# Optimization experiments

Hardware: AMD Instinct MI355X
Metric: run time of the kernel (lower is better)

Reference implementation:

```python
import jax, jax.numpy as jnp
import numpy as np

EPS = 1e-5


def _conv1x1(w, x):
    # w: [O, C, 1, 1], x: [B, C, H, W] -> [B, O, H, W]
    return jnp.einsum('oc,bchw->bohw', w[:, :, 0, 0], x)


def _bn_train(y, g, b):
    # BatchNorm2d in training mode: batch statistics over (B, H, W)
    m = y.mean(axis=(0, 2, 3), keepdims=True)
    v = y.var(axis=(0, 2, 3), keepdims=True)
    return (y - m) * jax.lax.rsqrt(v + EPS) * g[None, :, None, None] + b[None, :, None, None]


def setup_inputs() -> dict:
    key = jax.random.key(0)
    ks = jax.random.split(key, 8)
    B, C, H, W = 16, 512, 32, 32
    width, heads, hd, out_ch = 128, 4, 32, 512  # out_chans*expansion = 512
    return {
        'x': jax.random.normal(ks[0], (B, C, H, W), jnp.float32),
        'conv1_w': jax.random.normal(ks[1], (width, C, 1, 1), jnp.float32) * 0.05,
        'bn1_g': jnp.ones((width,), jnp.float32),
        'bn1_b': jnp.zeros((width,), jnp.float32),
        'qkv_w': jax.random.normal(ks[2], (3 * width, width, 1, 1), jnp.float32) * 0.05,
        'rw': jax.random.normal(ks[3], (1, heads, hd, 1, W), jnp.float32),
        'rh': jax.random.normal(ks[4], (1, heads, hd, H, 1), jnp.float32),
        'conv2_w': jax.random.normal(ks[5], (out_ch, width, 1, 1), jnp.float32) * 0.05,
        'bn2_g': jnp.ones((out_ch,), jnp.float32),
        'bn2_b': jnp.zeros((out_ch,), jnp.float32),
    }


def reference(x, conv1_w, bn1_g, bn1_b, qkv_w, rw, rh, conv2_w, bn2_g, bn2_b):
    B, C, H, W = x.shape
    heads = rw.shape[1]
    width = qkv_w.shape[1]
    hd = width // heads
    scale = hd ** (-0.5)
    N = H * W

    identity = x
    # conv1 = BaseConv: 1x1 conv (no bias) + BN + ReLU
    y = jax.nn.relu(_bn_train(_conv1x1(conv1_w, x), bn1_g, bn1_b))

    # Attention with relative position bias
    qkv = _conv1x1(qkv_w, y)                       # [B, 3*width, H, W]
    qkv = qkv.reshape(B, 3, heads, hd, N)          # split channels as (3, heads, hd)
    q, k, v = qkv[:, 0], qkv[:, 1], qkv[:, 2]      # each [B, heads, hd, N]

    attn_content = jnp.einsum('bhdn,bhdm->bhnm', q, k) * scale  # [B, heads, N, N]
    r = (rw + rh).reshape(heads, hd, N)                          # [heads, hd, N]
    attn_position = jnp.einsum('bhdn,hdm->bhnm', q, r) * scale
    attn = jax.nn.softmax(attn_content + attn_position, axis=-1)
    out = jnp.einsum('bhnm,bhdm->bhdn', attn, v)   # [B, heads, hd, N]
    y = out.reshape(B, width, H, W)

    # conv2 + BN, residual add, ReLU (stride==1: no pooling, no down_sample)
    y = _bn_train(_conv1x1(conv2_w, y), bn2_g, bn2_b)
    y = y + identity
    return jax.nn.relu(y)
```

## Files before the change

### kernel.cpp

```cpp
#include <hip/hip_runtime.h>
#include <cstddef>
#include <cstdint>

constexpr int BATCH = 16;
constexpr int NQ    = 1024;
constexpr float QSCALE = 0.17677669529663687f * 1.4426950408889634f;

typedef __attribute__((ext_vector_type(8))) short bf8;
typedef __attribute__((ext_vector_type(4))) float f32x4;
typedef __attribute__((ext_vector_type(2))) unsigned short us2;
typedef __attribute__((ext_vector_type(4))) unsigned short us4;
typedef __attribute__((ext_vector_type(8))) unsigned short us8;

__device__ inline unsigned short f2bf(float x) {
  union { float f; uint32_t u; } c{x};
  uint32_t r = c.u + 0x7fffu + ((c.u >> 16) & 1u);
  return (unsigned short)(r >> 16);
}
__device__ inline float b2f(unsigned short v) {
  union { uint32_t u; float f; } c{(uint32_t)v << 16};
  return c.f;
}
__device__ inline float fast_exp2(float x) {
#if __has_builtin(__builtin_amdgcn_exp2f)
  return __builtin_amdgcn_exp2f(x);
#else
  return exp2f(x);
#endif
}

__global__ __launch_bounds__(256) void k_wcvt(const float* __restrict__ w1,
                                              const float* __restrict__ wq,
                                              const float* __restrict__ w2,
                                              unsigned short* __restrict__ o1,
                                              unsigned short* __restrict__ oq,
                                              unsigned short* __restrict__ o2) {
  int idx = (blockIdx.x * 256 + threadIdx.x) * 8;
  const float* s; unsigned short* d; int off;
  if (idx < 65536)        { s = w1; d = o1; off = idx; }
  else if (idx < 114688)  { s = wq; d = oq; off = idx - 65536; }
  else                    { s = w2; d = o2; off = idx - 114688; }
  float4 a = *(const float4*)(s + off);
  float4 b = *(const float4*)(s + off + 4);
  us8 o = {f2bf(a.x), f2bf(a.y), f2bf(a.z), f2bf(a.w),
           f2bf(b.x), f2bf(b.y), f2bf(b.z), f2bf(b.w)};
  *(us8*)(d + off) = o;
}

__global__ __launch_bounds__(256) void k_conv1(const float* __restrict__ x,
                                               const unsigned short* __restrict__ W,
                                               unsigned short* __restrict__ y1T,
                                               float* __restrict__ pS1,
                                               float* __restrict__ pQ1) {
  constexpr int BS = 68;
  __shared__ unsigned short Bl[32 * BS];
  __shared__ float Sl[128], Ql[128];

  const int bb = blockIdx.z;
  const int n0 = blockIdx.x * 32;
  const int tid = threadIdx.x, lane = tid & 63;
  const int wm = tid >> 6;
  const int i = lane & 15, g = lane >> 4;

  const int kb = tid >> 3;
  const int nb = tid & 7;

  f32x4 acc[2][2];
#pragma unroll
  for (int a = 0; a < 2; ++a)
#pragma unroll
    for (int b = 0; b < 2; ++b) acc[a][b] = {0.f, 0.f, 0.f, 0.f};

  float4 rv[2];
#pragma unroll
  for (int r = 0; r < 2; ++r)
    rv[r] = *(const float4*)(x + (((size_t)(bb * 512 + kb * 2 + r)) << 10) + n0 + nb * 4);

  for (int s = 0; s < 8; ++s) {
    bf8 wf[2][2];
#pragma unroll
    for (int b = 0; b < 2; ++b)
#pragma unroll
      for (int h = 0; h < 2; ++h)
        wf[b][h] = *(const bf8*)(W + (size_t)(wm * 32 + b * 16 + i) * 512 + s * 64 + h * 32 + g * 8);

    __syncthreads();
#pragma unroll
    for (int j = 0; j < 4; ++j) {
      us2 pk = {f2bf((&rv[0].x)[j]), f2bf((&rv[1].x)[j])};
      *(us2*)&Bl[(nb * 4 + j) * BS + kb * 2] = pk;
    }
    __syncthreads();

    if (s < 7) {
#pragma unroll
      for (int r = 0; r < 2; ++r)
        rv[r] = *(const float4*)(x + (((size_t)(bb * 512 + (s + 1) * 64 + kb * 2 + r)) << 10) + n0 + nb * 4);
    }

#pragma unroll
    for (int h = 0; h < 2; ++h) {
      bf8 af[2];
#pragma unroll
      for (int a = 0; a < 2; ++a)
        af[a] = *(const bf8*)&Bl[(a * 16 + i) * BS + h * 32 + g * 8];
#pragma unroll
      for (int a = 0; a < 2; ++a)
#pragma unroll
        for (int b = 0; b < 2; ++b)
          acc[a][b] = __builtin_amdgcn_mfma_f32_16x16x32_bf16(wf[b][h], af[a], acc[a][b], 0, 0, 0);
    }
  }

#pragma unroll
  for (int a = 0; a < 2; ++a)
#pragma unroll
    for (int b = 0; b < 2; ++b) {
      const int n = n0 + a * 16 + i;
      const int c = wm * 32 + b * 16 + 4 * g;
      us4 pk = {f2bf(acc[a][b][0]), f2bf(acc[a][b][1]), f2bf(acc[a][b][2]), f2bf(acc[a][b][3])};
      *(us4*)(y1T + ((size_t)(bb << 10) + n) * 128 + c) = pk;
    }

#pragma unroll
  for (int b = 0; b < 2; ++b) {
    float sb[4], qb[4];
#pragma unroll
    for (int r = 0; r < 4; ++r) {
      float v0 = b2f(f2bf(acc[0][b][r]));
      float v1 = b2f(f2bf(acc[1][b][r]));
      sb[r] = v0 + v1;
      qb[r] = v0 * v0 + v1 * v1;
    }
#pragma unroll
    for (int o = 1; o < 16; o <<= 1) {
#pragma unroll
      for (int r = 0; r < 4; ++r) {
        sb[r] += __shfl_xor(sb[r], o);
        qb[r] += __shfl_xor(qb[r], o);
      }
    }
    if (i == 0) {
#pragma unroll
      for (int r = 0; r < 4; ++r) {
        const int c = wm * 32 + b * 16 + 4 * g + r;
        Sl[c] = sb[r];
        Ql[c] = qb[r];
      }
    }
  }

  __syncthreads();
  const int blk = bb * 32 + blockIdx.x;
  if (tid < 128) {
    pS1[(size_t)tid * 512 + blk] = Sl[tid];
    pQ1[(size_t)tid * 512 + blk] = Ql[tid];
  }
}

__global__ __launch_bounds__(64) void k_bnfin1(const float* __restrict__ pS1,
                                               const float* __restrict__ pQ1,
                                               const float* __restrict__ g,
                                               const float* __restrict__ be,
                                               float* __restrict__ scl,
                                               float* __restrict__ sht) {
  const int c = blockIdx.x, t = threadIdx.x;
  float S = 0.f, Q = 0.f;
#pragma unroll
  for (int k = 0; k < 8; ++k) {
    S += pS1[(size_t)c * 512 + t + k * 64];
    Q += pQ1[(size_t)c * 512 + t + k * 64];
  }
#pragma unroll
  for (int o = 32; o > 0; o >>= 1) {
    S += __shfl_down(S, o);
    Q += __shfl_down(Q, o);
  }
  if (t == 0) {
    const float inv_n = 1.f / 16384.f;
    const float mean = S * inv_n, var = Q * inv_n - mean * mean;
    const float sc = rsqrtf(var + 1e-5f) * g[c];
    scl[c] = sc;
    sht[c] = be[c] - mean * sc;
  }
}

__global__ __launch_bounds__(256) void k_qkv(const unsigned short* __restrict__ W,
                                             const unsigned short* __restrict__ Bact,
                                             const float* __restrict__ scl,
                                             const float* __restrict__ sht,
                                             const float* __restrict__ rw,
                                             const float* __restrict__ rh,
                                             unsigned short* __restrict__ out0,
                                             unsigned short* __restrict__ out1,
                                             unsigned short* __restrict__ out2) {
  constexpr int BS = 136;
  __shared__ unsigned short Blds[128 * BS];
  __shared__ float scl_s[128], sht_s[128];

  const int bb = blockIdx.z, half = blockIdx.y;
  const int n0 = blockIdx.x * 128;
  const int tid = threadIdx.x, lane = tid & 63, wv = tid >> 6;
  const int wn = wv & 1, wm = wv >> 1;
  const int i = lane & 15, g = lane >> 4;

  const unsigned short* Bp = Bact + ((size_t)bb * NQ + n0) * 128;

  const int sn = tid >> 1;
  const int sk = (tid & 1) * 8;

  if (tid < 128) { scl_s[tid] = scl[tid]; sht_s[tid] = sht[tid]; }

  auto loadw = [&](bf8 (&wf)[2][4], int typ) {
    const int m0 = typ * 128 + half * 64;
#pragma unroll
    for (int b = 0; b < 2; ++b)
#pragma unroll
      for (int h = 0; h < 4; ++h)
        wf[b][h] = *(const bf8*)(W + (size_t)(m0 + wm * 32 + b * 16 + i) * 128 + h * 32 + g * 8);
  };

  bf8 wf0[2][4], wf1[2][4];
  loadw(wf0, 0);
  __syncthreads();

#pragma unroll
  for (int p = 0; p < 8; ++p) {
    us8 v = *(const us8*)(Bp + (size_t)sn * 128 + sk + p * 16);
    const int kb = sk + p * 16;
    float scv[8], shv[8];
    *(float4*)scv = *(const float4*)&scl_s[kb];
    *(float4*)(scv + 4) = *(const float4*)&scl_s[kb + 4];
    *(float4*)shv = *(const float4*)&sht_s[kb];
    *(float4*)(shv + 4) = *(const float4*)&sht_s[kb + 4];
#pragma unroll
    for (int j = 0; j < 8; ++j)
      v[j] = f2bf(fmaxf(fmaf(b2f(v[j]), scv[j], shv[j]), 0.f));
    *(us8*)(&Blds[sn * BS + sk + p * 16]) = v;
  }
  __syncthreads();

  f32x4 acc[4][2];

  auto gemmWA = [&](bf8 (&wf)[2][4]) {
#pragma unroll
    for (int a = 0; a < 4; ++a)
#pragma unroll
      for (int b = 0; b < 2; ++b) acc[a][b] = {0.f, 0.f, 0.f, 0.f};
#pragma unroll
    for (int h = 0; h < 4; ++h) {
      bf8 af[4];
#pragma unroll
      for (int a = 0; a < 4; ++a)
        af[a] = *(const bf8*)&Blds[(wn * 64 + a * 16 + i) * BS + h * 32 + g * 8];
#pragma unroll
      for (int a = 0; a < 4; ++a)
#pragma unroll
        for (int b = 0; b < 2; ++b)
          acc[a][b] = __builtin_amdgcn_mfma_f32_16x16x32_bf16(wf[b][h], af[a], acc[a][b], 0, 0, 0);
    }
  };
  auto gemmAW = [&](bf8 (&wf)[2][4]) {
#pragma unroll
    for (int a = 0; a < 4; ++a)
#pragma unroll
      for (int b = 0; b < 2; ++b) acc[a][b] = {0.f, 0.f, 0.f, 0.f};
#pragma unroll
    for (int h = 0; h < 4; ++h) {
      bf8 af[4];
#pragma unroll
      for (int a = 0; a < 4; ++a)
        af[a] = *(const bf8*)&Blds[(wn * 64 + a * 16 + i) * BS + h * 32 + g * 8];
#pragma unroll
      for (int a = 0; a < 4; ++a)
#pragma unroll
        for (int b = 0; b < 2; ++b)
          acc[a][b] = __builtin_amdgcn_mfma_f32_16x16x32_bf16(af[a], wf[b][h], acc[a][b], 0, 0, 0);
    }
  };

  loadw(wf1, 1);
  gemmWA(wf0);
#pragma unroll
  for (int a = 0; a < 4; ++a)
#pragma unroll
    for (int b = 0; b < 2; ++b) {
      const int n = n0 + wn * 64 + a * 16 + i;
      const int c = half * 64 + wm * 32 + b * 16 + 4 * g;
      const int hh = c >> 5, d = c & 31;
      us4 pk = {f2bf(acc[a][b][0] * QSCALE), f2bf(acc[a][b][1] * QSCALE),
                f2bf(acc[a][b][2] * QSCALE), f2bf(acc[a][b][3] * QSCALE)};
      *(us4*)(out0 + (((size_t)(bb * 4 + hh) << 10) + n) * 32 + d) = pk;
    }

  loadw(wf0, 2);
  gemmWA(wf1);
#pragma unroll
  for (int a = 0; a < 4; ++a)
#pragma unroll
    for (int b = 0; b < 2; ++b) {
      const int n = n0 + wn * 64 + a * 16 + i;
      const int c = half * 64 + wm * 32 + b * 16 + 4 * g;
      const int hh = c >> 5, d = c & 31;
      const int wcol = n & 31, hrow = n >> 5;
      float vv[4];
#pragma unroll
      for (int r = 0; r < 4; ++r)
        vv[r] = acc[a][b][r] + rw[(c + r) * 32 + wcol] + rh[(c + r) * 32 + hrow];
      us4 pk = {f2bf(vv[0]), f2bf(vv[1]), f2bf(vv[2]), f2bf(vv[3])};
      *(us4*)(out1 + (((size_t)(bb * 4 + hh) << 10) + n) * 32 + d) = pk;
    }

  gemmAW(wf0);
#pragma unroll
  for (int a = 0; a < 4; ++a)
#pragma unroll
    for (int b = 0; b < 2; ++b) {
      const int c = half * 64 + wm * 32 + b * 16 + i;
      const int nb = n0 + wn * 64 + a * 16 + 4 * g;
      const int hh = c >> 5, dd = c & 31;
      us4 pk = {f2bf(acc[a][b][0]), f2bf(acc[a][b][1]), f2bf(acc[a][b][2]), f2bf(acc[a][b][3])};
      *(us4*)(out2 + (((size_t)(bb * 4 + hh) * 32 + dd) << 10) + nb) = pk;
    }
}

__global__ __launch_bounds__(256) void k_attn_part(const unsigned short* __restrict__ qs,
                                                   const unsigned short* __restrict__ kt,
                                                   const unsigned short* __restrict__ vt,
                                                   float* __restrict__ po,
                                                   float* __restrict__ pm,
                                                   float* __restrict__ pl) {
  const int bh   = blockIdx.y;
  const int part = blockIdx.z;
  const int tid  = threadIdx.x;
  const int lane = tid & 63;
  const int wv   = tid >> 6;
  const int i    = lane & 15;
  const int g    = lane >> 4;
  const int n0w  = blockIdx.x * 128 + wv * 32;

  __shared__ unsigned short Ks[64 * 56];
  __shared__ unsigned short Vt[32 * 72];

  const bf8 qfA = *(const bf8*)(qs + ((size_t)bh * NQ + n0w + i) * 32 + g * 8);
  const bf8 qfB = *(const bf8*)(qs + ((size_t)bh * NQ + n0w + 16 + i) * 32 + g * 8);

  f32x4 o0A = {0.f,0.f,0.f,0.f}, o1A = {0.f,0.f,0.f,0.f};
  f32x4 o0B = {0.f,0.f,0.f,0.f}, o1B = {0.f,0.f,0.f,0.f};
  float mA = -1e30f, lA = 0.f, mB = -1e30f, lB = 0.f;

  const unsigned short* kb = kt + (size_t)bh * NQ * 32;
  const unsigned short* vb = vt + (size_t)bh * 32 * NQ;

  const int skey = tid >> 2, sds = (tid & 3) * 8;
  const int svd  = tid >> 3, svn = (tid & 7) * 8;

  const int kbeg = part * 512, kend = kbeg + 512;

  bf8 kvld = *(const bf8*)(kb + (size_t)(kbeg + skey) * 32 + sds);
  bf8 vvld = *(const bf8*)(vb + (size_t)svd * NQ + kbeg + svn);

  for (int k0 = kbeg; k0 < kend; k0 += 64) {
    __syncthreads();
    *(bf8*)&Ks[skey * 56 + sds] = kvld;
    *(bf8*)&Vt[svd * 72 + svn]  = vvld;
    __syncthreads();
    if (k0 + 64 < kend) {
      kvld = *(const bf8*)(kb + (size_t)(k0 + 64 + skey) * 32 + sds);
      vvld = *(const bf8*)(vb + (size_t)svd * NQ + (k0 + 64) + svn);
    }

    const f32x4 zero = {0.f,0.f,0.f,0.f};
    f32x4 stA[4], stB[4];
#pragma unroll
    for (int t = 0; t < 4; ++t) {
      bf8 kf = *(const bf8*)&Ks[(t * 16 + i) * 56 + g * 8];
      stA[t] = __builtin_amdgcn_mfma_f32_16x16x32_bf16(kf, qfA, zero, 0, 0, 0);
      stB[t] = __builtin_amdgcn_mfma_f32_16x16x32_bf16(kf, qfB, zero, 0, 0, 0);
    }

    unsigned int pkA[4][2], pkB[4][2];
    {
      float tmax = stA[0][0];
#pragma unroll
      for (int t = 0; t < 4; ++t)
#pragma unroll
        for (int r = 0; r < 4; ++r) tmax = fmaxf(tmax, stA[t][r]);
      tmax = fmaxf(tmax, __shfl_xor(tmax, 16));
      tmax = fmaxf(tmax, __shfl_xor(tmax, 32));
      const float mn = fmaxf(mA, tmax);
      const float corr = fast_exp2(mA - mn);
      mA = mn;
      float ps = 0.f;
#pragma unroll
      for (int t = 0; t < 4; ++t) {
        float p0 = fast_exp2(stA[t][0] - mn);
        float p1 = fast_exp2(stA[t][1] - mn);
        float p2 = fast_exp2(stA[t][2] - mn);
        float p3 = fast_exp2(stA[t][3] - mn);
        ps += (p0 + p1) + (p2 + p3);
        unsigned int pa, pb;
        asm("v_cvt_pk_bf16_f32 %0, %1, %2" : "=v"(pa) : "v"(p0), "v"(p1));
        asm("v_cvt_pk_bf16_f32 %0, %1, %2" : "=v"(pb) : "v"(p2), "v"(p3));
        pkA[t][0] = pa; pkA[t][1] = pb;
      }
      ps += __shfl_xor(ps, 16);
      ps += __shfl_xor(ps, 32);
      lA = lA * corr + ps;
#pragma unroll
      for (int r = 0; r < 4; ++r) { o0A[r] *= corr; o1A[r] *= corr; }
    }
    {
      float tmax = stB[0][0];
#pragma unroll
      for (int t = 0; t < 4; ++t)
#pragma unroll
        for (int r = 0; r < 4; ++r) tmax = fmaxf(tmax, stB[t][r]);
      tmax = fmaxf(tmax, __shfl_xor(tmax, 16));
      tmax = fmaxf(tmax, __shfl_xor(tmax, 32));
      const float mn = fmaxf(mB, tmax);
      const float corr = fast_exp2(mB - mn);
      mB = mn;
      float ps = 0.f;
#pragma unroll
      for (int t = 0; t < 4; ++t) {
        float p0 = fast_exp2(stB[t][0] - mn);
        float p1 = fast_exp2(stB[t][1] - mn);
        float p2 = fast_exp2(stB[t][2] - mn);
        float p3 = fast_exp2(stB[t][3] - mn);
        ps += (p0 + p1) + (p2 + p3);
        unsigned int pa, pb;
        asm("v_cvt_pk_bf16_f32 %0, %1, %2" : "=v"(pa) : "v"(p0), "v"(p1));
        asm("v_cvt_pk_bf16_f32 %0, %1, %2" : "=v"(pb) : "v"(p2), "v"(p3));
        pkB[t][0] = pa; pkB[t][1] = pb;
      }
      ps += __shfl_xor(ps, 16);
      ps += __shfl_xor(ps, 32);
      lB = lB * corr + ps;
#pragma unroll
      for (int r = 0; r < 4; ++r) { o0B[r] *= corr; o1B[r] *= corr; }
    }

    const int src0 = ((g & 1) << 5) + i;
    const int src1 = src0 + 16;
    const bool hi = (g >= 2);
#pragma unroll
    for (int s = 0; s < 2; ++s) {
      int a0 = __shfl((int)pkA[2 * s][0], src0);
      int a1 = __shfl((int)pkA[2 * s][1], src0);
      int a2 = __shfl((int)pkA[2 * s][0], src1);
      int a3 = __shfl((int)pkA[2 * s][1], src1);
      int b0 = __shfl((int)pkA[2 * s + 1][0], src0);
      int b1 = __shfl((int)pkA[2 * s + 1][1], src0);
      int b2 = __shfl((int)pkA[2 * s + 1][0], src1);
      int b3 = __shfl((int)pkA[2 * s + 1][1], src1);
      union { int d[4]; bf8 v; } pfA;
      pfA.d[0] = hi ? b0 : a0;
      pfA.d[1] = hi ? b1 : a1;
      pfA.d[2] = hi ? b2 : a2;
      pfA.d[3] = hi ? b3 : a3;
      int c0 = __shfl((int)pkB[2 * s][0], src0);
      int c1 = __shfl((int)pkB[2 * s][1], src0);
      int c2 = __shfl((int)pkB[2 * s][0], src1);
      int c3 = __shfl((int)pkB[2 * s][1], src1);
      int d0 = __shfl((int)pkB[2 * s + 1][0], src0);
      int d1 = __shfl((int)pkB[2 * s + 1][1], src0);
      int d2 = __shfl((int)pkB[2 * s + 1][0], src1);
      int d3 = __shfl((int)pkB[2 * s + 1][1], src1);
      union { int d[4]; bf8 v; } pfB;
      pfB.d[0] = hi ? d0 : c0;
      pfB.d[1] = hi ? d1 : c1;
      pfB.d[2] = hi ? d2 : c2;
      pfB.d[3] = hi ? d3 : c3;
      bf8 vf0 = *(const bf8*)&Vt[(i)      * 72 + s * 32 + g * 8];
      bf8 vf1 = *(const bf8*)&Vt[(16 + i) * 72 + s * 32 + g * 8];
      o0A = __builtin_amdgcn_mfma_f32_16x16x32_bf16(vf0, pfA.v, o0A, 0, 0, 0);
      o1A = __builtin_amdgcn_mfma_f32_16x16x32_bf16(vf1, pfA.v, o1A, 0, 0, 0);
      o0B = __builtin_amdgcn_mfma_f32_16x16x32_bf16(vf0, pfB.v, o0B, 0, 0, 0);
      o1B = __builtin_amdgcn_mfma_f32_16x16x32_bf16(vf1, pfB.v, o1B, 0, 0, 0);
    }
  }

  const size_t pb = ((size_t)(part * 64 + bh) << 10);
  float* dA = po + (pb + n0w + i) * 32 + 4 * g;
  float* dB = po + (pb + n0w + 16 + i) * 32 + 4 * g;
  *(f32x4*)dA        = o0A;
  *(f32x4*)(dA + 16) = o1A;
  *(f32x4*)dB        = o0B;
  *(f32x4*)(dB + 16) = o1B;
  if (g == 0) {
    pm[pb + n0w + i]      = mA;
    pl[pb + n0w + i]      = lA;
    pm[pb + n0w + 16 + i] = mB;
    pl[pb + n0w + 16 + i] = lB;
  }
}

__global__ __launch_bounds__(256) void k_attn_comb(const float* __restrict__ po,
                                                   const float* __restrict__ pm,
                                                   const float* __restrict__ pl,
                                                   float* __restrict__ aoT) {
  const int bh = blockIdx.y;
  const int q  = blockIdx.x * 64 + (threadIdx.x >> 2);
  const int dc = (threadIdx.x & 3) * 8;

  const size_t p0 = ((size_t)bh << 10) + q;
  const size_t p1 = ((size_t)(64 + bh) << 10) + q;

  const float m0 = pm[p0], m1 = pm[p1];
  const float l0 = pl[p0], l1 = pl[p1];
  const float M  = fmaxf(m0, m1);
  const float w0 = fast_exp2(m0 - M);
  const float w1 = fast_exp2(m1 - M);
  const float inv = 1.f / (w0 * l0 + w1 * l1);
  const float c0 = w0 * inv, c1 = w1 * inv;

  f32x4 a0 = *(const f32x4*)(po + p0 * 32 + dc);
  f32x4 a1 = *(const f32x4*)(po + p0 * 32 + dc + 4);
  f32x4 b0 = *(const f32x4*)(po + p1 * 32 + dc);
  f32x4 b1 = *(const f32x4*)(po + p1 * 32 + dc + 4);
  f32x4 o0, o1;
#pragma unroll
  for (int r = 0; r < 4; ++r) {
    o0[r] = a0[r] * c0 + b0[r] * c1;
    o1[r] = a1[r] * c0 + b1[r] * c1;
  }

  float* dst = aoT + (((size_t)(bh >> 2) << 10) + q) * 128 + (bh & 3) * 32 + dc;
  *(f32x4*)dst       = o0;
  *(f32x4*)(dst + 4) = o1;
}

__global__ __launch_bounds__(256) void k_stat2(const unsigned short* __restrict__ W,
                                               const float* __restrict__ Aof,
                                               float* __restrict__ pBS,
                                               float* __restrict__ pBQ) {
  constexpr int BS = 264;
  __shared__ unsigned short Blds[64 * BS];
  __shared__ float Sl[256], Ql[256];
  const int bb = blockIdx.z;
  const int mh = blockIdx.y;
  const int n0 = blockIdx.x * 64;
  const int tid = threadIdx.x, lane = tid & 63, wv = tid >> 6;
  const int wn = wv & 1, wm = wv >> 1;
  const int i = lane & 15, g = lane >> 4;

  Sl[tid] = 0.f; Ql[tid] = 0.f;

  const int sn = tid >> 2, sk = (tid & 3) * 32;
  const float* src = Aof + (((size_t)(bb << 10)) + n0 + sn) * 128 + sk;
#pragma unroll
  for (int p = 0; p < 4; ++p) {
    float4 f0 = *(const float4*)(src + p * 8);
    float4 f1 = *(const float4*)(src + p * 8 + 4);
    float fv[8] = {f0.x, f0.y, f0.z, f0.w, f1.x, f1.y, f1.z, f1.w};
    us8 hi, lo;
#pragma unroll
    for (int j = 0; j < 8; ++j) {
      unsigned short h16 = f2bf(fv[j]);
      hi[j] = h16;
      lo[j] = f2bf(fv[j] - b2f(h16));
    }
    *(us8*)&Blds[sn * BS + sk + p * 8]       = hi;
    *(us8*)&Blds[sn * BS + 128 + sk + p * 8] = lo;
  }
  __syncthreads();

  auto loadw = [&](bf8 (&wf)[2][4], int lp) {
    const int mt = mh * 4 + lp;
#pragma unroll
    for (int b = 0; b < 2; ++b)
#pragma unroll
      for (int h = 0; h < 4; ++h)
        wf[b][h] = *(const bf8*)(W + (size_t)(mt * 64 + wm * 32 + b * 16 + i) * 128 + h * 32 + g * 8);
  };

  auto step = [&](bf8 (&wf)[2][4], int lp) {
    f32x4 acc[2][2];
#pragma unroll
    for (int a = 0; a < 2; ++a)
#pragma unroll
      for (int b = 0; b < 2; ++b) acc[a][b] = {0.f, 0.f, 0.f, 0.f};
#pragma unroll
    for (int h = 0; h < 4; ++h) {
      bf8 ah[2], al[2];
#pragma unroll
      for (int a = 0; a < 2; ++a) {
        ah[a] = *(const bf8*)&Blds[(wn * 32 + a * 16 + i) * BS + h * 32 + g * 8];
        al[a] = *(const bf8*)&Blds[(wn * 32 + a * 16 + i) * BS + 128 + h * 32 + g * 8];
      }
#pragma unroll
      for (int a = 0; a < 2; ++a)
#pragma unroll
        for (int b = 0; b < 2; ++b) {
          acc[a][b] = __builtin_amdgcn_mfma_f32_16x16x32_bf16(ah[a], wf[b][h], acc[a][b], 0, 0, 0);
          acc[a][b] = __builtin_amdgcn_mfma_f32_16x16x32_bf16(al[a], wf[b][h], acc[a][b], 0, 0, 0);
        }
    }
#pragma unroll
    for (int b = 0; b < 2; ++b) {
      float s = 0.f, q = 0.f;
#pragma unroll
      for (int a = 0; a < 2; ++a)
#pragma unroll
        for (int r = 0; r < 4; ++r) {
          float v = acc[a][b][r];
          s += v; q += v * v;
        }
      s += __shfl_xor(s, 16); s += __shfl_xor(s, 32);
      q += __shfl_xor(q, 16); q += __shfl_xor(q, 32);
      if ((lane & 48) == 0) {
        const int cl = lp * 64 + wm * 32 + b * 16 + i;
        atomicAdd(&Sl[cl], s);
        atomicAdd(&Ql[cl], q);
      }
    }
  };

  bf8 wfA[2][4], wfB[2][4];
  loadw(wfA, 0);
  loadw(wfB, 1);
  step(wfA, 0);
  loadw(wfA, 2);
  step(wfB, 1);
  loadw(wfB, 3);
  step(wfA, 2);
  step(wfB, 3);

  __syncthreads();
  const int pidx = bb * 16 + blockIdx.x;
  pBS[(size_t)(mh * 256 + tid) * 256 + pidx] = Sl[tid];
  pBQ[(size_t)(mh * 256 + tid) * 256 + pidx] = Ql[tid];
}

__global__ __launch_bounds__(64) void k_bnfin2(const float* __restrict__ pBS,
                                               const float* __restrict__ pBQ,
                                               const float* __restrict__ g,
                                               const float* __restrict__ be,
                                               float* __restrict__ scl,
                                               float* __restrict__ sht) {
  const int c = blockIdx.x, t = threadIdx.x;
  float S = 0.f, Q = 0.f;
#pragma unroll
  for (int k = 0; k < 4; ++k) {
    S += pBS[(size_t)c * 256 + t + k * 64];
    Q += pBQ[(size_t)c * 256 + t + k * 64];
  }
#pragma unroll
  for (int o = 32; o > 0; o >>= 1) {
    S += __shfl_down(S, o);
    Q += __shfl_down(Q, o);
  }
  if (t == 0) {
    const float inv_n = 1.f / 16384.f;
    const float mean = S * inv_n, var = Q * inv_n - mean * mean;
    const float sc = rsqrtf(var + 1e-5f) * g[c];
    scl[c] = sc;
    sht[c] = be[c] - mean * sc;
  }
}

__global__ __launch_bounds__(256) void k_final2(const unsigned short* __restrict__ W,
                                                const float* __restrict__ Aof,
                                                const float* __restrict__ x,
                                                const float* __restrict__ scl2,
                                                const float* __restrict__ sht2,
                                                float* __restrict__ out) {
  constexpr int BS = 264;
  __shared__ unsigned short Blds[64 * BS];
  __shared__ float scl_s[256], sht_s[256];
  const int bb = blockIdx.z;
  const int mh = blockIdx.y;
  const int n0 = blockIdx.x * 64;
  const int tid = threadIdx.x, lane = tid & 63, wv = tid >> 6;
  const int wn = wv & 1, wm = wv >> 1;
  const int i = lane & 15, g = lane >> 4;

  scl_s[tid] = scl2[mh * 256 + tid];
  sht_s[tid] = sht2[mh * 256 + tid];

  const int sn = tid >> 2, sk = (tid & 3) * 32;
  const float* src = Aof + (((size_t)(bb << 10)) + n0 + sn) * 128 + sk;
#pragma unroll
  for (int p = 0; p < 4; ++p) {
    float4 f0 = *(const float4*)(src + p * 8);
    float4 f1 = *(const float4*)(src + p * 8 + 4);
    float fv[8] = {f0.x, f0.y, f0.z, f0.w, f1.x, f1.y, f1.z, f1.w};
    us8 hi, lo;
#pragma unroll
    for (int j = 0; j < 8; ++j) {
      unsigned short h16 = f2bf(fv[j]);
      hi[j] = h16;
      lo[j] = f2bf(fv[j] - b2f(h16));
    }
    *(us8*)&Blds[sn * BS + sk + p * 8]       = hi;
    *(us8*)&Blds[sn * BS + 128 + sk + p * 8] = lo;
  }
  __syncthreads();

  auto loadw = [&](bf8 (&wf)[2][4], int lp) {
    const int mt = mh * 4 + lp;
#pragma unroll
    for (int b = 0; b < 2; ++b)
#pragma unroll
      for (int h = 0; h < 4; ++h)
        wf[b][h] = *(const bf8*)(W + (size_t)(mt * 64 + wm * 32 + b * 16 + i) * 128 + h * 32 + g * 8);
  };

  auto step = [&](bf8 (&wf)[2][4], int lp) {
    const int mt = mh * 4 + lp;
    f32x4 acc[2][2];
#pragma unroll
    for (int a = 0; a < 2; ++a)
#pragma unroll
      for (int b = 0; b < 2; ++b) acc[a][b] = {0.f, 0.f, 0.f, 0.f};
#pragma unroll
    for (int h = 0; h < 4; ++h) {
      bf8 ah[2], al[2];
#pragma unroll
      for (int a = 0; a < 2; ++a) {
        ah[a] = *(const bf8*)&Blds[(wn * 32 + a * 16 + i) * BS + h * 32 + g * 8];
        al[a] = *(const bf8*)&Blds[(wn * 32 + a * 16 + i) * BS + 128 + h * 32 + g * 8];
      }
#pragma unroll
      for (int a = 0; a < 2; ++a)
#pragma unroll
        for (int b = 0; b < 2; ++b) {
          acc[a][b] = __builtin_amdgcn_mfma_f32_16x16x32_bf16(ah[a], wf[b][h], acc[a][b], 0, 0, 0);
          acc[a][b] = __builtin_amdgcn_mfma_f32_16x16x32_bf16(al[a], wf[b][h], acc[a][b], 0, 0, 0);
        }
    }
#pragma unroll
    for (int a = 0; a < 2; ++a)
#pragma unroll
      for (int b = 0; b < 2; ++b) {
        const int c = mt * 64 + wm * 32 + b * 16 + i;
        const int cl = lp * 64 + wm * 32 + b * 16 + i;
        const int nb = n0 + wn * 32 + a * 16 + 4 * g;
        const float sc = scl_s[cl], sh = sht_s[cl];
        const size_t off = (((size_t)(bb * 512 + c)) << 10) + nb;
        float4 xv = *(const float4*)(x + off);
        f32x4 o;
        o[0] = fmaxf(acc[a][b][0] * sc + sh + xv.x, 0.f);
        o[1] = fmaxf(acc[a][b][1] * sc + sh + xv.y, 0.f);
        o[2] = fmaxf(acc[a][b][2] * sc + sh + xv.z, 0.f);
        o[3] = fmaxf(acc[a][b][3] * sc + sh + xv.w, 0.f);
        *(f32x4*)(out + off) = o;
      }
  };

  bf8 wfA[2][4], wfB[2][4];
  loadw(wfA, 0);
  loadw(wfB, 1);
  step(wfA, 0);
  loadw(wfA, 2);
  step(wfB, 1);
  loadw(wfB, 3);
  step(wfA, 2);
  step(wfB, 3);
}

extern "C" void kernel_launch(void* const* d_in, const int* in_sizes, int n_in,
                              void* d_out, int out_size, void* d_ws, size_t ws_size,
                              hipStream_t stream) {
  (void)in_sizes; (void)n_in; (void)out_size; (void)ws_size;
  const float* x    = (const float*)d_in[0];
  const float* w1   = (const float*)d_in[1];
  const float* g1   = (const float*)d_in[2];
  const float* b1   = (const float*)d_in[3];
  const float* wqkv = (const float*)d_in[4];
  const float* rw   = (const float*)d_in[5];
  const float* rh   = (const float*)d_in[6];
  const float* w2   = (const float*)d_in[7];
  const float* g2   = (const float*)d_in[8];
  const float* b2   = (const float*)d_in[9];
  float* out = (float*)d_out;
  char* base = (char*)d_ws;

  float*          aoT = (float*)(base);
  unsigned short* y1T = (unsigned short*)(base + (8u  << 20));
  unsigned short* qs  = (unsigned short*)(base + (12u << 20));
  unsigned short* kt  = (unsigned short*)(base + (16u << 20));
  unsigned short* vt  = (unsigned short*)(base + (20u << 20));
  unsigned short* wb1 = (unsigned short*)(base + (24u << 20));
  unsigned short* wbq = wb1 + 65536;
  unsigned short* wb2 = wbq + 49152;
  float* pS1  = (float*)(base + (25u << 20));
  float* pQ1  = pS1 + 65536;
  float* pBS  = pQ1 + 65536;
  float* pBQ  = pBS + 131072;
  float* scl1 = pBQ + 131072;
  float* sht1 = scl1 + 128;
  float* scl2 = sht1 + 128;
  float* sht2 = scl2 + 512;
  float* po   = (float*)(base + (32u << 20));
  float* pm   = (float*)(base + (48u << 20));
  float* pl   = pm + 131072;

  k_wcvt<<<88, 256, 0, stream>>>(w1, wqkv, w2, wb1, wbq, wb2);
  k_conv1<<<dim3(32, 1, BATCH), 256, 0, stream>>>(x, wb1, y1T, pS1, pQ1);
  k_bnfin1<<<128, 64, 0, stream>>>(pS1, pQ1, g1, b1, scl1, sht1);
  k_qkv<<<dim3(8, 2, BATCH), 256, 0, stream>>>(wbq, y1T, scl1, sht1,
                                               rw, rh, qs, kt, vt);
  k_attn_part<<<dim3(NQ / 128, BATCH * 4, 2), 256, 0, stream>>>(qs, kt, vt, po, pm, pl);
  k_attn_comb<<<dim3(16, BATCH * 4), 256, 0, stream>>>(po, pm, pl, aoT);
  k_stat2<<<dim3(16, 2, BATCH), 256, 0, stream>>>(wb2, aoT, pBS, pBQ);
  k_bnfin2<<<512, 64, 0, stream>>>(pBS, pBQ, g2, b2, scl2, sht2);
  k_final2<<<dim3(16, 2, BATCH), 256, 0, stream>>>(wb2, aoT, x, scl2, sht2, out);
}
```

Measured before the change: 103.3 us.

## Double-buffer K/V tiles in attention and fuse split-combine into conv2 kernels

```diff
diff --git a/kernel.cpp b/kernel.cpp
--- a/kernel.cpp
+++ b/kernel.cpp
@@ -339,8 +339,8 @@
   const int g    = lane >> 4;
   const int n0w  = blockIdx.x * 128 + wv * 32;
 
-  __shared__ unsigned short Ks[64 * 56];
-  __shared__ unsigned short Vt[32 * 72];
+  __shared__ unsigned short Ks[2][64 * 56];
+  __shared__ unsigned short Vt[2][32 * 72];
 
   const bf8 qfA = *(const bf8*)(qs + ((size_t)bh * NQ + n0w + i) * 32 + g * 8);
   const bf8 qfB = *(const bf8*)(qs + ((size_t)bh * NQ + n0w + 16 + i) * 32 + g * 8);
@@ -355,29 +355,32 @@
   const int skey = tid >> 2, sds = (tid & 3) * 8;
   const int svd  = tid >> 3, svn = (tid & 7) * 8;
 
-  const int kbeg = part * 512, kend = kbeg + 512;
+  const int kbeg = part * 512;
 
   bf8 kvld = *(const bf8*)(kb + (size_t)(kbeg + skey) * 32 + sds);
   bf8 vvld = *(const bf8*)(vb + (size_t)svd * NQ + kbeg + svn);
-
-  for (int k0 = kbeg; k0 < kend; k0 += 64) {
-    __syncthreads();
-    *(bf8*)&Ks[skey * 56 + sds] = kvld;
-    *(bf8*)&Vt[svd * 72 + svn]  = vvld;
-    __syncthreads();
-    if (k0 + 64 < kend) {
-      kvld = *(const bf8*)(kb + (size_t)(k0 + 64 + skey) * 32 + sds);
-      vvld = *(const bf8*)(vb + (size_t)svd * NQ + (k0 + 64) + svn);
+  *(bf8*)&Ks[0][skey * 56 + sds] = kvld;
+  *(bf8*)&Vt[0][svd * 72 + svn]  = vvld;
+  __syncthreads();
+
+  for (int it = 0; it < 8; ++it) {
+    const int cur = it & 1, nxt = cur ^ 1;
+    if (it < 7) {
+      const int k0n = kbeg + (it + 1) * 64;
+      kvld = *(const bf8*)(kb + (size_t)(k0n + skey) * 32 + sds);
+      vvld = *(const bf8*)(vb + (size_t)svd * NQ + k0n + svn);
     }
 
     const f32x4 zero = {0.f,0.f,0.f,0.f};
     f32x4 stA[4], stB[4];
+    __builtin_amdgcn_s_setprio(1);
 #pragma unroll
     for (int t = 0; t < 4; ++t) {
-      bf8 kf = *(const bf8*)&Ks[(t * 16 + i) * 56 + g * 8];
+      bf8 kf = *(const bf8*)&Ks[cur][(t * 16 + i) * 56 + g * 8];
       stA[t] = __builtin_amdgcn_mfma_f32_16x16x32_bf16(kf, qfA, zero, 0, 0, 0);
       stB[t] = __builtin_amdgcn_mfma_f32_16x16x32_bf16(kf, qfB, zero, 0, 0, 0);
     }
+    __builtin_amdgcn_s_setprio(0);
 
     unsigned int pkA[4][2], pkB[4][2];
     {
@@ -444,6 +447,7 @@
     const int src0 = ((g & 1) << 5) + i;
     const int src1 = src0 + 16;
     const bool hi = (g >= 2);
+    __builtin_amdgcn_s_setprio(1);
 #pragma unroll
     for (int s = 0; s < 2; ++s) {
       int a0 = __shfl((int)pkA[2 * s][0], src0);
@@ -472,13 +476,20 @@
       pfB.d[1] = hi ? d1 : c1;
       pfB.d[2] = hi ? d2 : c2;
       pfB.d[3] = hi ? d3 : c3;
-      bf8 vf0 = *(const bf8*)&Vt[(i)      * 72 + s * 32 + g * 8];
-      bf8 vf1 = *(const bf8*)&Vt[(16 + i) * 72 + s * 32 + g * 8];
+      bf8 vf0 = *(const bf8*)&Vt[cur][(i)      * 72 + s * 32 + g * 8];
+      bf8 vf1 = *(const bf8*)&Vt[cur][(16 + i) * 72 + s * 32 + g * 8];
       o0A = __builtin_amdgcn_mfma_f32_16x16x32_bf16(vf0, pfA.v, o0A, 0, 0, 0);
       o1A = __builtin_amdgcn_mfma_f32_16x16x32_bf16(vf1, pfA.v, o1A, 0, 0, 0);
       o0B = __builtin_amdgcn_mfma_f32_16x16x32_bf16(vf0, pfB.v, o0B, 0, 0, 0);
       o1B = __builtin_amdgcn_mfma_f32_16x16x32_bf16(vf1, pfB.v, o1B, 0, 0, 0);
     }
+    __builtin_amdgcn_s_setprio(0);
+
+    if (it < 7) {
+      *(bf8*)&Ks[nxt][skey * 56 + sds] = kvld;
+      *(bf8*)&Vt[nxt][svd * 72 + svn]  = vvld;
+    }
+    __syncthreads();
   }
 
   const size_t pb = ((size_t)(part * 64 + bh) << 10);
@@ -496,43 +507,10 @@
   }
 }
 
-__global__ __launch_bounds__(256) void k_attn_comb(const float* __restrict__ po,
-                                                   const float* __restrict__ pm,
-                                                   const float* __restrict__ pl,
-                                                   float* __restrict__ aoT) {
-  const int bh = blockIdx.y;
-  const int q  = blockIdx.x * 64 + (threadIdx.x >> 2);
-  const int dc = (threadIdx.x & 3) * 8;
-
-  const size_t p0 = ((size_t)bh << 10) + q;
-  const size_t p1 = ((size_t)(64 + bh) << 10) + q;
-
-  const float m0 = pm[p0], m1 = pm[p1];
-  const float l0 = pl[p0], l1 = pl[p1];
-  const float M  = fmaxf(m0, m1);
-  const float w0 = fast_exp2(m0 - M);
-  const float w1 = fast_exp2(m1 - M);
-  const float inv = 1.f / (w0 * l0 + w1 * l1);
-  const float c0 = w0 * inv, c1 = w1 * inv;
-
-  f32x4 a0 = *(const f32x4*)(po + p0 * 32 + dc);
-  f32x4 a1 = *(const f32x4*)(po + p0 * 32 + dc + 4);
-  f32x4 b0 = *(const f32x4*)(po + p1 * 32 + dc);
-  f32x4 b1 = *(const f32x4*)(po + p1 * 32 + dc + 4);
-  f32x4 o0, o1;
-#pragma unroll
-  for (int r = 0; r < 4; ++r) {
-    o0[r] = a0[r] * c0 + b0[r] * c1;
-    o1[r] = a1[r] * c0 + b1[r] * c1;
-  }
-
-  float* dst = aoT + (((size_t)(bh >> 2) << 10) + q) * 128 + (bh & 3) * 32 + dc;
-  *(f32x4*)dst       = o0;
-  *(f32x4*)(dst + 4) = o1;
-}
-
 __global__ __launch_bounds__(256) void k_stat2(const unsigned short* __restrict__ W,
-                                               const float* __restrict__ Aof,
+                                               const float* __restrict__ po,
+                                               const float* __restrict__ pm,
+                                               const float* __restrict__ pl,
                                                float* __restrict__ pBS,
                                                float* __restrict__ pBQ) {
   constexpr int BS = 264;
@@ -547,22 +525,43 @@
 
   Sl[tid] = 0.f; Ql[tid] = 0.f;
 
-  const int sn = tid >> 2, sk = (tid & 3) * 32;
-  const float* src = Aof + (((size_t)(bb << 10)) + n0 + sn) * 128 + sk;
-#pragma unroll
-  for (int p = 0; p < 4; ++p) {
-    float4 f0 = *(const float4*)(src + p * 8);
-    float4 f1 = *(const float4*)(src + p * 8 + 4);
-    float fv[8] = {f0.x, f0.y, f0.z, f0.w, f1.x, f1.y, f1.z, f1.w};
-    us8 hi, lo;
-#pragma unroll
-    for (int j = 0; j < 8; ++j) {
-      unsigned short h16 = f2bf(fv[j]);
-      hi[j] = h16;
-      lo[j] = f2bf(fv[j] - b2f(h16));
-    }
-    *(us8*)&Blds[sn * BS + sk + p * 8]       = hi;
-    *(us8*)&Blds[sn * BS + 128 + sk + p * 8] = lo;
+  {
+    const int sn = tid >> 2, sk = (tid & 3) * 32;
+    const int h  = tid & 3;
+    const int n  = n0 + sn;
+    const size_t q0 = (((size_t)(bb * 4 + h)) << 10) + n;
+    const size_t q1 = (((size_t)(64 + bb * 4 + h)) << 10) + n;
+    const float m0 = pm[q0], m1 = pm[q1];
+    const float l0 = pl[q0], l1 = pl[q1];
+    const float M  = fmaxf(m0, m1);
+    const float w0 = fast_exp2(m0 - M);
+    const float w1 = fast_exp2(m1 - M);
+    const float inv = 1.f / (w0 * l0 + w1 * l1);
+    const float c0 = w0 * inv, c1 = w1 * inv;
+    const float* s0 = po + q0 * 32;
+    const float* s1 = po + q1 * 32;
+#pragma unroll
+    for (int p = 0; p < 4; ++p) {
+      f32x4 a0 = *(const f32x4*)(s0 + p * 8);
+      f32x4 a1 = *(const f32x4*)(s0 + p * 8 + 4);
+      f32x4 b0 = *(const f32x4*)(s1 + p * 8);
+      f32x4 b1 = *(const f32x4*)(s1 + p * 8 + 4);
+      float fv[8];
+#pragma unroll
+      for (int r = 0; r < 4; ++r) {
+        fv[r]     = a0[r] * c0 + b0[r] * c1;
+        fv[4 + r] = a1[r] * c0 + b1[r] * c1;
+      }
+      us8 hi, lo;
+#pragma unroll
+      for (int j = 0; j < 8; ++j) {
+        unsigned short h16 = f2bf(fv[j]);
+        hi[j] = h16;
+        lo[j] = f2bf(fv[j] - b2f(h16));
+      }
+      *(us8*)&Blds[sn * BS + sk + p * 8]       = hi;
+      *(us8*)&Blds[sn * BS + 128 + sk + p * 8] = lo;
+    }
   }
   __syncthreads();
 
@@ -661,7 +660,9 @@
 }
 
 __global__ __launch_bounds__(256) void k_final2(const unsigned short* __restrict__ W,
-                                                const float* __restrict__ Aof,
+                                                const float* __restrict__ po,
+                                                const float* __restrict__ pm,
+                                                const float* __restrict__ pl,
                                                 const float* __restrict__ x,
                                                 const float* __restrict__ scl2,
                                                 const float* __restrict__ sht2,
@@ -679,22 +680,43 @@
   scl_s[tid] = scl2[mh * 256 + tid];
   sht_s[tid] = sht2[mh * 256 + tid];
 
-  const int sn = tid >> 2, sk = (tid & 3) * 32;
-  const float* src = Aof + (((size_t)(bb << 10)) + n0 + sn) * 128 + sk;
-#pragma unroll
-  for (int p = 0; p < 4; ++p) {
-    float4 f0 = *(const float4*)(src + p * 8);
-    float4 f1 = *(const float4*)(src + p * 8 + 4);
-    float fv[8] = {f0.x, f0.y, f0.z, f0.w, f1.x, f1.y, f1.z, f1.w};
-    us8 hi, lo;
-#pragma unroll
-    for (int j = 0; j < 8; ++j) {
-      unsigned short h16 = f2bf(fv[j]);
-      hi[j] = h16;
-      lo[j] = f2bf(fv[j] - b2f(h16));
-    }
-    *(us8*)&Blds[sn * BS + sk + p * 8]       = hi;
-    *(us8*)&Blds[sn * BS + 128 + sk + p * 8] = lo;
+  {
+    const int sn = tid >> 2, sk = (tid & 3) * 32;
+    const int h  = tid & 3;
+    const int n  = n0 + sn;
+    const size_t q0 = (((size_t)(bb * 4 + h)) << 10) + n;
+    const size_t q1 = (((size_t)(64 + bb * 4 + h)) << 10) + n;
+    const float m0 = pm[q0], m1 = pm[q1];
+    const float l0 = pl[q0], l1 = pl[q1];
+    const float M  = fmaxf(m0, m1);
+    const float w0 = fast_exp2(m0 - M);
+    const float w1 = fast_exp2(m1 - M);
+    const float inv = 1.f / (w0 * l0 + w1 * l1);
+    const float c0 = w0 * inv, c1 = w1 * inv;
+    const float* s0 = po + q0 * 32;
+    const float* s1 = po + q1 * 32;
+#pragma unroll
+    for (int p = 0; p < 4; ++p) {
+      f32x4 a0 = *(const f32x4*)(s0 + p * 8);
+      f32x4 a1 = *(const f32x4*)(s0 + p * 8 + 4);
+      f32x4 b0 = *(const f32x4*)(s1 + p * 8);
+      f32x4 b1 = *(const f32x4*)(s1 + p * 8 + 4);
+      float fv[8];
+#pragma unroll
+      for (int r = 0; r < 4; ++r) {
+        fv[r]     = a0[r] * c0 + b0[r] * c1;
+        fv[4 + r] = a1[r] * c0 + b1[r] * c1;
+      }
+      us8 hi, lo;
+#pragma unroll
+      for (int j = 0; j < 8; ++j) {
+        unsigned short h16 = f2bf(fv[j]);
+        hi[j] = h16;
+        lo[j] = f2bf(fv[j] - b2f(h16));
+      }
+      *(us8*)&Blds[sn * BS + sk + p * 8]       = hi;
+      *(us8*)&Blds[sn * BS + 128 + sk + p * 8] = lo;
+    }
   }
   __syncthreads();
 
@@ -777,7 +799,6 @@
   float* out = (float*)d_out;
   char* base = (char*)d_ws;
 
-  float*          aoT = (float*)(base);
   unsigned short* y1T = (unsigned short*)(base + (8u  << 20));
   unsigned short* qs  = (unsigned short*)(base + (12u << 20));
   unsigned short* kt  = (unsigned short*)(base + (16u << 20));
@@ -803,8 +824,7 @@
   k_qkv<<<dim3(8, 2, BATCH), 256, 0, stream>>>(wbq, y1T, scl1, sht1,
                                                rw, rh, qs, kt, vt);
   k_attn_part<<<dim3(NQ / 128, BATCH * 4, 2), 256, 0, stream>>>(qs, kt, vt, po, pm, pl);
-  k_attn_comb<<<dim3(16, BATCH * 4), 256, 0, stream>>>(po, pm, pl, aoT);
-  k_stat2<<<dim3(16, 2, BATCH), 256, 0, stream>>>(wb2, aoT, pBS, pBQ);
+  k_stat2<<<dim3(16, 2, BATCH), 256, 0, stream>>>(wb2, po, pm, pl, pBS, pBQ);
   k_bnfin2<<<512, 64, 0, stream>>>(pBS, pBQ, g2, b2, scl2, sht2);
-  k_final2<<<dim3(16, 2, BATCH), 256, 0, stream>>>(wb2, aoT, x, scl2, sht2, out);
-}
+  k_final2<<<dim3(16, 2, BATCH), 256, 0, stream>>>(wb2, po, pm, pl, x, scl2, sht2, out);
+}
```

Result: no change. 104.3 us (+1.0%).
